# Performance work log

Measured on AMD Instinct MI355X. Metric: run time of the kernel, lower is better.

## Reference

```python
import jax, jax.numpy as jnp
import numpy as np

E = 8       # num experts
T = 1024    # num tokens
H = 1024    # hidden dim
I = 1024    # intermediate dim (per gate/up half)


def setup_inputs() -> dict:
    key = jax.random.key(0)
    k1, k2, k3, k4 = jax.random.split(key, 4)
    return {
        "hidden_states": jax.random.normal(k1, (T, H), jnp.float32),
        "router_logits": jax.random.normal(k2, (T, E), jnp.float32),
        # W13 stored pre-transposed as in the module: [E, H, 2*I]
        "W13": jax.random.normal(k3, (E, H, 2 * I), jnp.float32) * 0.02,
        # W2 stored pre-transposed: [E, I, H]
        "W2": jax.random.normal(k4, (E, I, H), jnp.float32) * 0.02,
        "top_k": 2,
    }


def reference(hidden_states, router_logits, W13, W2, top_k):
    num_experts = router_logits.shape[-1]
    # --- routing: topk_softmax (softmax over all experts, then top-k) ---
    probs = jax.nn.softmax(router_logits, axis=-1)            # [T, E]
    w, idx = jax.lax.top_k(probs, top_k)                      # [T, K]
    # renormalize=True path of moe_gather
    w = w / jnp.sum(w, axis=-1, keepdims=True)
    # combine weights per expert: [T, E]
    combine = jnp.sum(jax.nn.one_hot(idx, num_experts, dtype=w.dtype) * w[..., None], axis=1)
    # --- grouped gate-up GEMM + silu_and_mul ---
    h13 = jnp.einsum('th,ehf->tef', hidden_states, W13)       # [T, E, 2I]
    gate, up = jnp.split(h13, 2, axis=-1)                     # each [T, E, I]
    act = jax.nn.silu(gate) * up                              # silu_and_mul
    # --- grouped down GEMM ---
    down = jnp.einsum('tei,eih->teh', act, W2)                # [T, E, H]
    # --- combine (moe_gather) ---
    return jnp.einsum('te,teh->th', combine, down)            # [T, H]
```

## Files before the change

kernel.cpp:

```cpp
#include <hip/hip_runtime.h>
#include <stdint.h>

#define NE    8
#define NTOK  1024
#define NH    1024
#define NI    1024
#define N13   2048

#define PREP_BLOCKS 513
#define G1MAX       1248
#define G2MAX       1248

typedef __attribute__((ext_vector_type(8))) short short8;
typedef __attribute__((ext_vector_type(4))) float f32x4;
typedef unsigned short u16;
typedef unsigned int   u32;

__device__ __forceinline__ u16 f2bf(float x) {
    union { float f; u32 u; } v; v.f = x;
    return (u16)((v.u + 0x7fffu + ((v.u >> 16) & 1u)) >> 16);
}
__device__ __forceinline__ u32 pack2(float a, float b) {
    return (u32)f2bf(a) | ((u32)f2bf(b) << 16);
}
__device__ __forceinline__ u32 cvt_pk(float lo, float hi) {
    u32 r;
    asm("v_cvt_pk_bf16_f32 %0, %1, %2" : "=v"(r) : "v"(lo), "v"(hi));
    return r;
}
__device__ __forceinline__ void async_ld16(u16* lds, const u16* g) {
    __builtin_amdgcn_global_load_lds(
        (const __attribute__((address_space(1))) u32*)g,
        (__attribute__((address_space(3))) u32*)lds, 16, 0, 0);
}

__device__ __forceinline__ bool find_tile(
    const int* __restrict__ counts, int tile, int bm, int ntn,
    int& e_o, int& mt_o, int& nt_o, int& cnt_o, int& base_o)
{
    int base = 0;
    #pragma unroll
    for (int e = 0; e < NE; e++) {
        const int cnt = counts[e];
        const int mtiles = (cnt + bm - 1) / bm;
        const int tiles = mtiles * ntn;
        if (tile < tiles) {
            e_o = e; mt_o = tile / ntn; nt_o = tile - (tile / ntn) * ntn;
            cnt_o = cnt; base_o = base; return true;
        }
        tile -= tiles; base += cnt;
    }
    return false;
}

#define SYNCV(N)                                                           \
    {                                                                      \
        asm volatile("s_waitcnt vmcnt(" #N ") lgkmcnt(0)" ::: "memory");   \
        __builtin_amdgcn_s_barrier();                                      \
        __builtin_amdgcn_sched_barrier(0);                                 \
    }

__global__ __launch_bounds__(256) void prep_kernel(
    const float* __restrict__ X, const float* __restrict__ logits,
    int* __restrict__ counts, int* __restrict__ pair_tok,
    int* __restrict__ inv, float* __restrict__ tokw,
    u16* __restrict__ Xb)
{
    __shared__ int s_cnt[NE];
    __shared__ int s_base[NE];
    const int tid = threadIdx.x;
    const int b = blockIdx.x;

    if (b == 0) {
        if (tid < NE) s_cnt[tid] = 0;
        __syncthreads();
        int eA[4][2]; int slotA[4][2]; float wA[4][2];
        #pragma unroll
        for (int i = 0; i < 4; i++) {
            const int t = tid * 4 + i;
            float l[NE];
            #pragma unroll
            for (int e = 0; e < NE; e++) l[e] = logits[t * NE + e];
            int i0 = 0;
            #pragma unroll
            for (int e = 1; e < NE; e++) if (l[e] > l[i0]) i0 = e;
            int i1 = -1;
            #pragma unroll
            for (int e = 0; e < NE; e++) {
                if (e == i0) continue;
                if (i1 < 0 || l[e] > l[i1]) i1 = e;
            }
            const float e10 = __expf(l[i1] - l[i0]);
            const float invw = 1.0f / (1.0f + e10);
            eA[i][0] = i0; eA[i][1] = i1;
            wA[i][0] = invw; wA[i][1] = e10 * invw;
            slotA[i][0] = atomicAdd(&s_cnt[i0], 1);
            slotA[i][1] = atomicAdd(&s_cnt[i1], 1);
        }
        __syncthreads();
        if (tid == 0) {
            int acc = 0;
            #pragma unroll
            for (int e = 0; e < NE; e++) { s_base[e] = acc; acc += s_cnt[e]; }
        }
        __syncthreads();
        if (tid < NE) counts[tid] = s_cnt[tid];
        #pragma unroll
        for (int i = 0; i < 4; i++) {
            const int t = tid * 4 + i;
            #pragma unroll
            for (int k = 0; k < 2; k++) {
                const int p = s_base[eA[i][k]] + slotA[i][k];
                pair_tok[p] = t;
                inv[t * 2 + k] = p;
                tokw[t * 2 + k] = wA[i][k];
            }
        }
    } else {
        const int i = (b - 1) * 256 + tid;
        const float4* s = (const float4*)X;
        const float4 a = s[2 * i], c = s[2 * i + 1];
        uint4 o;
        o.x = pack2(a.x, a.y);
        o.y = pack2(a.z, a.w);
        o.z = pack2(c.x, c.y);
        o.w = pack2(c.z, c.w);
        *(uint4*)(Xb + (size_t)i * 8) = o;
    }
}

__global__ __launch_bounds__(256, 4) void gemm1_kernel(
    const u16* __restrict__ Xb, const float* __restrict__ W13,
    const int* __restrict__ counts, const int* __restrict__ pair_tok,
    u16* __restrict__ act)
{
    int e, mt, nt, cnt, base;
    if (!find_tile(counts, blockIdx.x, 64, 32, e, mt, nt, cnt, base)) return;

    __shared__ __align__(16) u16 As[3][64 * 32];
    __shared__ __align__(16) u16 Bs[3][64 * 40];

    const int tid = threadIdx.x;
    const int ct  = nt * 32;

    const int csrc = (((tid & 3) ^ ((tid >> 3) & 3)) << 3);
    const int arow = mt * 64 + (tid >> 2);
    const int tok  = pair_tok[base + min(arow, cnt - 1)];
    const u16* ga  = Xb + (size_t)tok * NH + csrc;

    const int n0 = (tid & 15) << 2;
    const int kp = tid >> 4;
    const int kc = kp >> 2;
    const int f0 = (n0 < 32) ? (ct + n0) : (NI + ct + n0 - 32);
    const float* gw = W13 + ((size_t)e * NH + 2 * kp) * N13 + f0;
    int wboff[4];
    #pragma unroll
    for (int jj = 0; jj < 4; jj++) {
        const int n = n0 + jj;
        wboff[jj] = n * 40 + ((kc ^ ((n >> 3) & 3)) << 3) + ((kp & 3) << 1);
    }

    const int lane = tid & 63, w = tid >> 6;
    const int quad = lane >> 4, lid = lane & 15;
    const int rw = w >> 1, cw = w & 1;
    int aoff[2];
    #pragma unroll
    for (int mi = 0; mi < 2; mi++) {
        const int r = rw * 32 + mi * 16 + lid;
        aoff[mi] = r * 32 + ((quad ^ ((r >> 1) & 3)) << 3);
    }
    int bgoff, buoff;
    { const int n = cw * 16 + lid;
      bgoff = n * 40 + ((quad ^ ((n >> 3) & 3)) << 3); }
    { const int n = 32 + cw * 16 + lid;
      buoff = n * 40 + ((quad ^ ((n >> 3) & 3)) << 3); }

    f32x4 accg[2] = {};
    f32x4 accu[2] = {};
    float4 bq[3][2];

#define ISSUEA1(S, K) async_ld16(&As[S][tid * 8], ga + (K));
#define LOADB1(RB, K)                                                      \
    { bq[RB][0] = *(const float4*)(gw + (size_t)(K) * N13);                \
      bq[RB][1] = *(const float4*)(gw + (size_t)(K) * N13 + N13); }
#define WRB1(S)                                                            \
    { _Pragma("unroll") for (int jj = 0; jj < 4; jj++) {                   \
        *(u32*)&Bs[S][wboff[jj]] =                                         \
            cvt_pk(((const float*)&bq[S][0])[jj],                          \
                   ((const float*)&bq[S][1])[jj]);                         \
    } }
#define COMP1(S)                                                           \
    {                                                                      \
        const short8 gv = *(const short8*)&Bs[S][bgoff];                   \
        const short8 uv = *(const short8*)&Bs[S][buoff];                   \
        __builtin_amdgcn_s_setprio(1);                                     \
        _Pragma("unroll") for (int mi = 0; mi < 2; mi++) {                 \
            const short8 av = *(const short8*)&As[S][aoff[mi]];            \
            accg[mi] = __builtin_amdgcn_mfma_f32_16x16x32_bf16(            \
                av, gv, accg[mi], 0, 0, 0);                                \
            accu[mi] = __builtin_amdgcn_mfma_f32_16x16x32_bf16(            \
                av, uv, accu[mi], 0, 0, 0);                                \
        }                                                                  \
        __builtin_amdgcn_s_setprio(0);                                     \
    }
#define G1_STEP(J, NV)                                                     \
    SYNCV(NV)                                                              \
    if ((J) + 2 < 32) { ISSUEA1((((J) + 2) % 3), (((J) + 2) * 32)) }       \
    if ((J) + 3 < 32) { LOADB1(((J) % 3), (((J) + 3) * 32)) }              \
    COMP1(((J) % 3))                                                       \
    if ((J) + 1 < 32) { WRB1((((J) + 1) % 3)) }

    LOADB1(0, 0)
    ISSUEA1(0, 0)
    LOADB1(1, 32)
    ISSUEA1(1, 32)
    LOADB1(2, 64)
    asm volatile("s_waitcnt vmcnt(6)" ::: "memory");
    WRB1(0)

    G1_STEP(0, 3)  G1_STEP(1, 3)  G1_STEP(2, 3)  G1_STEP(3, 3)
    G1_STEP(4, 3)  G1_STEP(5, 3)  G1_STEP(6, 3)  G1_STEP(7, 3)
    G1_STEP(8, 3)  G1_STEP(9, 3)  G1_STEP(10, 3) G1_STEP(11, 3)
    G1_STEP(12, 3) G1_STEP(13, 3) G1_STEP(14, 3) G1_STEP(15, 3)
    G1_STEP(16, 3) G1_STEP(17, 3) G1_STEP(18, 3) G1_STEP(19, 3)
    G1_STEP(20, 3) G1_STEP(21, 3) G1_STEP(22, 3) G1_STEP(23, 3)
    G1_STEP(24, 3) G1_STEP(25, 3) G1_STEP(26, 3) G1_STEP(27, 3)
    G1_STEP(28, 3) G1_STEP(29, 3) G1_STEP(30, 1) G1_STEP(31, 0)

    const int col = ct + cw * 16 + lid;
    #pragma unroll
    for (int mi = 0; mi < 2; mi++) {
        #pragma unroll
        for (int r = 0; r < 4; r++) {
            const int row = mt * 64 + rw * 32 + mi * 16 + quad * 4 + r;
            if (row < cnt) {
                const float g = accg[mi][r], u = accu[mi][r];
                act[(size_t)(base + row) * NI + col] =
                    f2bf(g / (1.0f + __expf(-g)) * u);
            }
        }
    }
#undef ISSUEA1
#undef LOADB1
#undef WRB1
#undef COMP1
#undef G1_STEP
}

__global__ __launch_bounds__(256, 4) void gemm2_kernel(
    const u16* __restrict__ act, const float* __restrict__ W2,
    const int* __restrict__ counts,
    float* __restrict__ down0, float* __restrict__ down1)
{
    int e, mt, ntq, cnt, base;
    if (!find_tile(counts, blockIdx.x, 64, 32, e, mt, ntq, cnt, base)) return;
    const int kh = ntq & 1;
    const int nt = ntq >> 1;
    const int ct = nt * 64;
    const int kbase = kh * 512;
    float* __restrict__ dwn = kh ? down1 : down0;

    __shared__ __align__(16) u16 As[3][64 * 32];
    __shared__ __align__(16) u16 Bs[3][64 * 40];

    const int tid = threadIdx.x;

    const int csrc = (((tid & 3) ^ ((tid >> 3) & 3)) << 3);
    const int arow = mt * 64 + (tid >> 2);
    const int p    = base + min(arow, cnt - 1);
    const u16* ga  = act + (size_t)p * NI + kbase + csrc;

    const int n0 = (tid & 15) << 2;
    const int kp = tid >> 4;
    const int kc = kp >> 2;
    const float* gw = W2 + ((size_t)e * NI + kbase + 2 * kp) * NH + ct + n0;
    int wboff[4];
    #pragma unroll
    for (int jj = 0; jj < 4; jj++) {
        const int n = n0 + jj;
        wboff[jj] = n * 40 + ((kc ^ ((n >> 3) & 3)) << 3) + ((kp & 3) << 1);
    }

    const int lane = tid & 63, w = tid >> 6;
    const int quad = lane >> 4, lid = lane & 15;
    const int rw = w >> 1, cw = w & 1;
    int aoff[2], boff[2];
    #pragma unroll
    for (int mi = 0; mi < 2; mi++) {
        const int r = rw * 32 + mi * 16 + lid;
        aoff[mi] = r * 32 + ((quad ^ ((r >> 1) & 3)) << 3);
    }
    #pragma unroll
    for (int nj = 0; nj < 2; nj++) {
        const int n = cw * 32 + nj * 16 + lid;
        boff[nj] = n * 40 + ((quad ^ ((n >> 3) & 3)) << 3);
    }

    f32x4 acc[2][2] = {};
    float4 bq[3][2];

#define ISSUEA2(S, K) async_ld16(&As[S][tid * 8], ga + (K));
#define LOADB2(RB, K)                                                      \
    { bq[RB][0] = *(const float4*)(gw + (size_t)(K) * NH);                 \
      bq[RB][1] = *(const float4*)(gw + (size_t)(K) * NH + NH); }
#define WRB2(S)                                                            \
    { _Pragma("unroll") for (int jj = 0; jj < 4; jj++) {                   \
        *(u32*)&Bs[S][wboff[jj]] =                                         \
            cvt_pk(((const float*)&bq[S][0])[jj],                          \
                   ((const float*)&bq[S][1])[jj]);                         \
    } }
#define COMP2(S)                                                           \
    {                                                                      \
        const short8 bv0 = *(const short8*)&Bs[S][boff[0]];                \
        const short8 bv1 = *(const short8*)&Bs[S][boff[1]];                \
        __builtin_amdgcn_s_setprio(1);                                     \
        _Pragma("unroll") for (int mi = 0; mi < 2; mi++) {                 \
            const short8 av = *(const short8*)&As[S][aoff[mi]];            \
            acc[mi][0] = __builtin_amdgcn_mfma_f32_16x16x32_bf16(          \
                av, bv0, acc[mi][0], 0, 0, 0);                             \
            acc[mi][1] = __builtin_amdgcn_mfma_f32_16x16x32_bf16(          \
                av, bv1, acc[mi][1], 0, 0, 0);                             \
        }                                                                  \
        __builtin_amdgcn_s_setprio(0);                                     \
    }
#define G2_STEP(J, NV)                                                     \
    SYNCV(NV)                                                              \
    if ((J) + 2 < 16) { ISSUEA2((((J) + 2) % 3), (((J) + 2) * 32)) }       \
    if ((J) + 3 < 16) { LOADB2(((J) % 3), (((J) + 3) * 32)) }              \
    COMP2(((J) % 3))                                                       \
    if ((J) + 1 < 16) { WRB2((((J) + 1) % 3)) }

    LOADB2(0, 0)
    ISSUEA2(0, 0)
    LOADB2(1, 32)
    ISSUEA2(1, 32)
    LOADB2(2, 64)
    asm volatile("s_waitcnt vmcnt(6)" ::: "memory");
    WRB2(0)

    G2_STEP(0, 3)  G2_STEP(1, 3)  G2_STEP(2, 3)  G2_STEP(3, 3)
    G2_STEP(4, 3)  G2_STEP(5, 3)  G2_STEP(6, 3)  G2_STEP(7, 3)
    G2_STEP(8, 3)  G2_STEP(9, 3)  G2_STEP(10, 3) G2_STEP(11, 3)
    G2_STEP(12, 3) G2_STEP(13, 3) G2_STEP(14, 1) G2_STEP(15, 0)

    #pragma unroll
    for (int mi = 0; mi < 2; mi++) {
        #pragma unroll
        for (int r = 0; r < 4; r++) {
            const int row = mt * 64 + rw * 32 + mi * 16 + quad * 4 + r;
            if (row < cnt) {
                #pragma unroll
                for (int nj = 0; nj < 2; nj++) {
                    dwn[(size_t)(base + row) * NH + ct + cw * 32 + nj * 16 + lid] =
                        acc[mi][nj][r];
                }
            }
        }
    }
#undef ISSUEA2
#undef LOADB2
#undef WRB2
#undef COMP2
#undef G2_STEP
}

__global__ __launch_bounds__(256) void combine_kernel(
    const float* __restrict__ down0, const float* __restrict__ down1,
    const int* __restrict__ inv, const float* __restrict__ tokw,
    float* __restrict__ out)
{
    const int t = blockIdx.x;
    const int p0 = inv[2 * t], p1 = inv[2 * t + 1];
    const float w0 = tokw[2 * t], w1 = tokw[2 * t + 1];
    const int i = threadIdx.x * 4;
    const float4 a0 = *(const float4*)(down0 + (size_t)p0 * NH + i);
    const float4 a1 = *(const float4*)(down1 + (size_t)p0 * NH + i);
    const float4 b0 = *(const float4*)(down0 + (size_t)p1 * NH + i);
    const float4 b1 = *(const float4*)(down1 + (size_t)p1 * NH + i);
    float4 o;
    o.x = w0 * (a0.x + a1.x) + w1 * (b0.x + b1.x);
    o.y = w0 * (a0.y + a1.y) + w1 * (b0.y + b1.y);
    o.z = w0 * (a0.z + a1.z) + w1 * (b0.z + b1.z);
    o.w = w0 * (a0.w + a1.w) + w1 * (b0.w + b1.w);
    *(float4*)(out + (size_t)t * NH + i) = o;
}

extern "C" void kernel_launch(void* const* d_in, const int* in_sizes, int n_in,
                              void* d_out, int out_size, void* d_ws, size_t ws_size,
                              hipStream_t stream)
{
    const float* X      = (const float*)d_in[0];
    const float* logits = (const float*)d_in[1];
    const float* W13    = (const float*)d_in[2];
    const float* W2     = (const float*)d_in[3];
    float* out = (float*)d_out;

    char* ws = (char*)d_ws;
    int*   counts   = (int*)(ws + 0);
    int*   pair_tok = (int*)(ws + 1024);
    int*   inv      = (int*)(ws + 16384);
    float* tokw     = (float*)(ws + 32768);
    u16*   Xb       = (u16*)(ws + 65536);
    u16*   act      = (u16*)(ws + (size_t)4  * 1024 * 1024);
    float* down0    = (float*)(ws + (size_t)8  * 1024 * 1024);
    float* down1    = (float*)(ws + (size_t)16 * 1024 * 1024);

    prep_kernel<<<PREP_BLOCKS, 256, 0, stream>>>(
        X, logits, counts, pair_tok, inv, tokw, Xb);
    gemm1_kernel<<<G1MAX, 256, 0, stream>>>(Xb, W13, counts, pair_tok, act);
    gemm2_kernel<<<G2MAX, 256, 0, stream>>>(act, W2, counts, down0, down1);
    combine_kernel<<<NTOK, 256, 0, stream>>>(down0, down1, inv, tokw, out);
}
```

Before: 187.6 us.

## Pre-convert weights to transposed bf16 in prep and stream them with async LDS loads

The prep kernel gains 6144 blocks that transpose W13 and W2 through shared memory into bf16 [E,N,K] buffers in the workspace. The GEMMs then load B tiles with global_load_lds directly, with no register-staged fp32 loads or in-loop conversion. The M tile grows from 64 to 128 rows and the pipeline deepens to four stages. Weight conversion is still done on every call, so fp32 weights are read once and bf16 copies are written and then re-read, which adds an extra pass over the weights.

Result: faster. 171.7 us (-8.4%).

```diff
diff --git a/kernel.cpp b/kernel.cpp
--- a/kernel.cpp
+++ b/kernel.cpp
@@ -7,9 +7,9 @@
 #define NI    1024
 #define N13   2048
 
-#define PREP_BLOCKS 513
-#define G1MAX       1248
-#define G2MAX       1248
+#define PREP_BLOCKS 6657
+#define G1MAX       768
+#define G2MAX       768
 
 typedef __attribute__((ext_vector_type(8))) short short8;
 typedef __attribute__((ext_vector_type(4))) float f32x4;
@@ -19,9 +19,6 @@
 __device__ __forceinline__ u16 f2bf(float x) {
     union { float f; u32 u; } v; v.f = x;
     return (u16)((v.u + 0x7fffu + ((v.u >> 16) & 1u)) >> 16);
-}
-__device__ __forceinline__ u32 pack2(float a, float b) {
-    return (u32)f2bf(a) | ((u32)f2bf(b) << 16);
 }
 __device__ __forceinline__ u32 cvt_pk(float lo, float hi) {
     u32 r;
@@ -62,16 +59,18 @@
 
 __global__ __launch_bounds__(256) void prep_kernel(
     const float* __restrict__ X, const float* __restrict__ logits,
+    const float* __restrict__ W13, const float* __restrict__ W2,
     int* __restrict__ counts, int* __restrict__ pair_tok,
     int* __restrict__ inv, float* __restrict__ tokw,
-    u16* __restrict__ Xb)
-{
-    __shared__ int s_cnt[NE];
-    __shared__ int s_base[NE];
+    u16* __restrict__ Xb, u16* __restrict__ W13t, u16* __restrict__ W2t)
+{
+    __shared__ __align__(16) float Ts[64][65];
     const int tid = threadIdx.x;
     const int b = blockIdx.x;
 
     if (b == 0) {
+        int* s_cnt  = (int*)&Ts[0][0];
+        int* s_base = s_cnt + NE;
         if (tid < NE) s_cnt[tid] = 0;
         __syncthreads();
         int eA[4][2]; int slotA[4][2]; float wA[4][2];
@@ -116,85 +115,104 @@
                 tokw[t * 2 + k] = wA[i][k];
             }
         }
-    } else {
+    } else if (b <= 512) {
         const int i = (b - 1) * 256 + tid;
         const float4* s = (const float4*)X;
         const float4 a = s[2 * i], c = s[2 * i + 1];
         uint4 o;
-        o.x = pack2(a.x, a.y);
-        o.y = pack2(a.z, a.w);
-        o.z = pack2(c.x, c.y);
-        o.w = pack2(c.z, c.w);
+        o.x = cvt_pk(a.x, a.y);
+        o.y = cvt_pk(a.z, a.w);
+        o.z = cvt_pk(c.x, c.y);
+        o.w = cvt_pk(c.z, c.w);
         *(uint4*)(Xb + (size_t)i * 8) = o;
-    }
-}
-
-__global__ __launch_bounds__(256, 4) void gemm1_kernel(
-    const u16* __restrict__ Xb, const float* __restrict__ W13,
+    } else {
+        const int wb = b - 513;
+        const float* src; u16* dst; int K, N, tb;
+        if (wb < 4096) { src = W13; dst = W13t; K = NH; N = N13; tb = wb; }
+        else           { src = W2;  dst = W2t;  K = NI; N = NH;  tb = wb - 4096; }
+        const int ktiles = K >> 6, ntiles = N >> 6;
+        const int tpe = ktiles * ntiles;
+        const int e = tb / tpe;
+        const int rem = tb - e * tpe;
+        const int kt = rem / ntiles, ntl = rem - (rem / ntiles) * ntiles;
+        const float* sb = src + ((size_t)e * K + (size_t)kt * 64) * N + ntl * 64;
+        #pragma unroll
+        for (int i = 0; i < 4; i++) {
+            const int idx = tid + i * 256;
+            const int r = idx >> 4, c = (idx & 15) << 2;
+            const float4 v = *(const float4*)(sb + (size_t)r * N + c);
+            Ts[r][c + 0] = v.x; Ts[r][c + 1] = v.y;
+            Ts[r][c + 2] = v.z; Ts[r][c + 3] = v.w;
+        }
+        __syncthreads();
+        u16* db = dst + ((size_t)e * N + (size_t)ntl * 64) * K + kt * 64;
+        #pragma unroll
+        for (int i = 0; i < 2; i++) {
+            const int u = tid + i * 256;
+            const int n = u >> 3, k8 = (u & 7) << 3;
+            uint4 o;
+            o.x = cvt_pk(Ts[k8 + 0][n], Ts[k8 + 1][n]);
+            o.y = cvt_pk(Ts[k8 + 2][n], Ts[k8 + 3][n]);
+            o.z = cvt_pk(Ts[k8 + 4][n], Ts[k8 + 5][n]);
+            o.w = cvt_pk(Ts[k8 + 6][n], Ts[k8 + 7][n]);
+            *(uint4*)(db + (size_t)n * K + k8) = o;
+        }
+    }
+}
+
+__global__ __launch_bounds__(256, 3) void gemm1_kernel(
+    const u16* __restrict__ Xb, const u16* __restrict__ W13t,
     const int* __restrict__ counts, const int* __restrict__ pair_tok,
     u16* __restrict__ act)
 {
     int e, mt, nt, cnt, base;
-    if (!find_tile(counts, blockIdx.x, 64, 32, e, mt, nt, cnt, base)) return;
-
-    __shared__ __align__(16) u16 As[3][64 * 32];
-    __shared__ __align__(16) u16 Bs[3][64 * 40];
+    if (!find_tile(counts, blockIdx.x, 128, 32, e, mt, nt, cnt, base)) return;
+
+    __shared__ __align__(16) u16 As[4][128 * 32];
+    __shared__ __align__(16) u16 Bs[4][64 * 32];
 
     const int tid = threadIdx.x;
     const int ct  = nt * 32;
 
-    const int csrc = (((tid & 3) ^ ((tid >> 3) & 3)) << 3);
-    const int arow = mt * 64 + (tid >> 2);
-    const int tok  = pair_tok[base + min(arow, cnt - 1)];
-    const u16* ga  = Xb + (size_t)tok * NH + csrc;
-
-    const int n0 = (tid & 15) << 2;
-    const int kp = tid >> 4;
-    const int kc = kp >> 2;
-    const int f0 = (n0 < 32) ? (ct + n0) : (NI + ct + n0 - 32);
-    const float* gw = W13 + ((size_t)e * NH + 2 * kp) * N13 + f0;
-    int wboff[4];
-    #pragma unroll
-    for (int jj = 0; jj < 4; jj++) {
-        const int n = n0 + jj;
-        wboff[jj] = n * 40 + ((kc ^ ((n >> 3) & 3)) << 3) + ((kp & 3) << 1);
-    }
+    const int sc = (((tid & 3) ^ ((tid >> 3) & 3)) << 3);
+    const int rr = tid >> 2;
+    const int tok0 = pair_tok[base + min(mt * 128 + rr,      cnt - 1)];
+    const int tok1 = pair_tok[base + min(mt * 128 + 64 + rr, cnt - 1)];
+    const u16* ga0 = Xb + (size_t)tok0 * NH + sc;
+    const u16* ga1 = Xb + (size_t)tok1 * NH + sc;
+    const int wcol = (rr < 32) ? (ct + rr) : (NI + ct + rr - 32);
+    const u16* gb  = W13t + ((size_t)e * N13 + wcol) * NH + sc;
 
     const int lane = tid & 63, w = tid >> 6;
     const int quad = lane >> 4, lid = lane & 15;
     const int rw = w >> 1, cw = w & 1;
-    int aoff[2];
-    #pragma unroll
-    for (int mi = 0; mi < 2; mi++) {
-        const int r = rw * 32 + mi * 16 + lid;
-        aoff[mi] = r * 32 + ((quad ^ ((r >> 1) & 3)) << 3);
+    int aoff[4];
+    #pragma unroll
+    for (int mi = 0; mi < 4; mi++) {
+        const int row = rw * 64 + mi * 16 + lid;
+        aoff[mi] = row * 32 + ((quad ^ ((row >> 1) & 3)) << 3);
     }
     int bgoff, buoff;
     { const int n = cw * 16 + lid;
-      bgoff = n * 40 + ((quad ^ ((n >> 3) & 3)) << 3); }
+      bgoff = n * 32 + ((quad ^ ((n >> 1) & 3)) << 3); }
     { const int n = 32 + cw * 16 + lid;
-      buoff = n * 40 + ((quad ^ ((n >> 3) & 3)) << 3); }
-
-    f32x4 accg[2] = {};
-    f32x4 accu[2] = {};
-    float4 bq[3][2];
-
-#define ISSUEA1(S, K) async_ld16(&As[S][tid * 8], ga + (K));
-#define LOADB1(RB, K)                                                      \
-    { bq[RB][0] = *(const float4*)(gw + (size_t)(K) * N13);                \
-      bq[RB][1] = *(const float4*)(gw + (size_t)(K) * N13 + N13); }
-#define WRB1(S)                                                            \
-    { _Pragma("unroll") for (int jj = 0; jj < 4; jj++) {                   \
-        *(u32*)&Bs[S][wboff[jj]] =                                         \
-            cvt_pk(((const float*)&bq[S][0])[jj],                          \
-                   ((const float*)&bq[S][1])[jj]);                         \
-    } }
+      buoff = n * 32 + ((quad ^ ((n >> 1) & 3)) << 3); }
+
+    f32x4 accg[4] = {};
+    f32x4 accu[4] = {};
+
+#define STAGE1(S, K)                                                       \
+    {                                                                      \
+        async_ld16(&As[S][tid * 8],         ga0 + (K));                    \
+        async_ld16(&As[S][(256 + tid) * 8], ga1 + (K));                    \
+        async_ld16(&Bs[S][tid * 8],         gb  + (K));                    \
+    }
 #define COMP1(S)                                                           \
     {                                                                      \
         const short8 gv = *(const short8*)&Bs[S][bgoff];                   \
         const short8 uv = *(const short8*)&Bs[S][buoff];                   \
         __builtin_amdgcn_s_setprio(1);                                     \
-        _Pragma("unroll") for (int mi = 0; mi < 2; mi++) {                 \
+        _Pragma("unroll") for (int mi = 0; mi < 4; mi++) {                 \
             const short8 av = *(const short8*)&As[S][aoff[mi]];            \
             accg[mi] = __builtin_amdgcn_mfma_f32_16x16x32_bf16(            \
                 av, gv, accg[mi], 0, 0, 0);                                \
@@ -203,36 +221,30 @@
         }                                                                  \
         __builtin_amdgcn_s_setprio(0);                                     \
     }
-#define G1_STEP(J, NV)                                                     \
+#define STEP1(J, NV)                                                       \
     SYNCV(NV)                                                              \
-    if ((J) + 2 < 32) { ISSUEA1((((J) + 2) % 3), (((J) + 2) * 32)) }       \
-    if ((J) + 3 < 32) { LOADB1(((J) % 3), (((J) + 3) * 32)) }              \
-    COMP1(((J) % 3))                                                       \
-    if ((J) + 1 < 32) { WRB1((((J) + 1) % 3)) }
-
-    LOADB1(0, 0)
-    ISSUEA1(0, 0)
-    LOADB1(1, 32)
-    ISSUEA1(1, 32)
-    LOADB1(2, 64)
-    asm volatile("s_waitcnt vmcnt(6)" ::: "memory");
-    WRB1(0)
-
-    G1_STEP(0, 3)  G1_STEP(1, 3)  G1_STEP(2, 3)  G1_STEP(3, 3)
-    G1_STEP(4, 3)  G1_STEP(5, 3)  G1_STEP(6, 3)  G1_STEP(7, 3)
-    G1_STEP(8, 3)  G1_STEP(9, 3)  G1_STEP(10, 3) G1_STEP(11, 3)
-    G1_STEP(12, 3) G1_STEP(13, 3) G1_STEP(14, 3) G1_STEP(15, 3)
-    G1_STEP(16, 3) G1_STEP(17, 3) G1_STEP(18, 3) G1_STEP(19, 3)
-    G1_STEP(20, 3) G1_STEP(21, 3) G1_STEP(22, 3) G1_STEP(23, 3)
-    G1_STEP(24, 3) G1_STEP(25, 3) G1_STEP(26, 3) G1_STEP(27, 3)
-    G1_STEP(28, 3) G1_STEP(29, 3) G1_STEP(30, 1) G1_STEP(31, 0)
+    if ((J) + 3 < 32) { STAGE1((((J) + 3) & 3), (((J) + 3) * 32)) }        \
+    COMP1(((J) & 3))
+
+    STAGE1(0, 0)
+    STAGE1(1, 32)
+    STAGE1(2, 64)
+
+    STEP1(0, 6)  STEP1(1, 6)  STEP1(2, 6)  STEP1(3, 6)
+    STEP1(4, 6)  STEP1(5, 6)  STEP1(6, 6)  STEP1(7, 6)
+    STEP1(8, 6)  STEP1(9, 6)  STEP1(10, 6) STEP1(11, 6)
+    STEP1(12, 6) STEP1(13, 6) STEP1(14, 6) STEP1(15, 6)
+    STEP1(16, 6) STEP1(17, 6) STEP1(18, 6) STEP1(19, 6)
+    STEP1(20, 6) STEP1(21, 6) STEP1(22, 6) STEP1(23, 6)
+    STEP1(24, 6) STEP1(25, 6) STEP1(26, 6) STEP1(27, 6)
+    STEP1(28, 6) STEP1(29, 6) STEP1(30, 3) STEP1(31, 0)
 
     const int col = ct + cw * 16 + lid;
     #pragma unroll
-    for (int mi = 0; mi < 2; mi++) {
+    for (int mi = 0; mi < 4; mi++) {
         #pragma unroll
         for (int r = 0; r < 4; r++) {
-            const int row = mt * 64 + rw * 32 + mi * 16 + quad * 4 + r;
+            const int row = mt * 128 + rw * 64 + mi * 16 + quad * 4 + r;
             if (row < cnt) {
                 const float g = accg[mi][r], u = accu[mi][r];
                 act[(size_t)(base + row) * NI + col] =
@@ -240,81 +252,66 @@
             }
         }
     }
-#undef ISSUEA1
-#undef LOADB1
-#undef WRB1
+#undef STAGE1
 #undef COMP1
-#undef G1_STEP
-}
-
-__global__ __launch_bounds__(256, 4) void gemm2_kernel(
-    const u16* __restrict__ act, const float* __restrict__ W2,
+#undef STEP1
+}
+
+__global__ __launch_bounds__(256, 3) void gemm2_kernel(
+    const u16* __restrict__ act, const u16* __restrict__ W2t,
     const int* __restrict__ counts,
     float* __restrict__ down0, float* __restrict__ down1)
 {
     int e, mt, ntq, cnt, base;
-    if (!find_tile(counts, blockIdx.x, 64, 32, e, mt, ntq, cnt, base)) return;
+    if (!find_tile(counts, blockIdx.x, 128, 32, e, mt, ntq, cnt, base)) return;
     const int kh = ntq & 1;
     const int nt = ntq >> 1;
     const int ct = nt * 64;
     const int kbase = kh * 512;
     float* __restrict__ dwn = kh ? down1 : down0;
 
-    __shared__ __align__(16) u16 As[3][64 * 32];
-    __shared__ __align__(16) u16 Bs[3][64 * 40];
+    __shared__ __align__(16) u16 As[4][128 * 32];
+    __shared__ __align__(16) u16 Bs[4][64 * 32];
 
     const int tid = threadIdx.x;
 
-    const int csrc = (((tid & 3) ^ ((tid >> 3) & 3)) << 3);
-    const int arow = mt * 64 + (tid >> 2);
-    const int p    = base + min(arow, cnt - 1);
-    const u16* ga  = act + (size_t)p * NI + kbase + csrc;
-
-    const int n0 = (tid & 15) << 2;
-    const int kp = tid >> 4;
-    const int kc = kp >> 2;
-    const float* gw = W2 + ((size_t)e * NI + kbase + 2 * kp) * NH + ct + n0;
-    int wboff[4];
-    #pragma unroll
-    for (int jj = 0; jj < 4; jj++) {
-        const int n = n0 + jj;
-        wboff[jj] = n * 40 + ((kc ^ ((n >> 3) & 3)) << 3) + ((kp & 3) << 1);
-    }
+    const int sc = (((tid & 3) ^ ((tid >> 3) & 3)) << 3);
+    const int rr = tid >> 2;
+    const int p0 = base + min(mt * 128 + rr,      cnt - 1);
+    const int p1 = base + min(mt * 128 + 64 + rr, cnt - 1);
+    const u16* ga0 = act + (size_t)p0 * NI + kbase + sc;
+    const u16* ga1 = act + (size_t)p1 * NI + kbase + sc;
+    const u16* gb  = W2t + ((size_t)e * NH + ct + rr) * NI + kbase + sc;
 
     const int lane = tid & 63, w = tid >> 6;
     const int quad = lane >> 4, lid = lane & 15;
     const int rw = w >> 1, cw = w & 1;
-    int aoff[2], boff[2];
-    #pragma unroll
-    for (int mi = 0; mi < 2; mi++) {
-        const int r = rw * 32 + mi * 16 + lid;
-        aoff[mi] = r * 32 + ((quad ^ ((r >> 1) & 3)) << 3);
+    int aoff[4], boff[2];
+    #pragma unroll
+    for (int mi = 0; mi < 4; mi++) {
+        const int row = rw * 64 + mi * 16 + lid;
+        aoff[mi] = row * 32 + ((quad ^ ((row >> 1) & 3)) << 3);
     }
     #pragma unroll
     for (int nj = 0; nj < 2; nj++) {
         const int n = cw * 32 + nj * 16 + lid;
-        boff[nj] = n * 40 + ((quad ^ ((n >> 3) & 3)) << 3);
-    }
-
-    f32x4 acc[2][2] = {};
-    float4 bq[3][2];
-
-#define ISSUEA2(S, K) async_ld16(&As[S][tid * 8], ga + (K));
-#define LOADB2(RB, K)                                                      \
-    { bq[RB][0] = *(const float4*)(gw + (size_t)(K) * NH);                 \
-      bq[RB][1] = *(const float4*)(gw + (size_t)(K) * NH + NH); }
-#define WRB2(S)                                                            \
-    { _Pragma("unroll") for (int jj = 0; jj < 4; jj++) {                   \
-        *(u32*)&Bs[S][wboff[jj]] =                                         \
-            cvt_pk(((const float*)&bq[S][0])[jj],                          \
-                   ((const float*)&bq[S][1])[jj]);                         \
-    } }
+        boff[nj] = n * 32 + ((quad ^ ((n >> 1) & 3)) << 3);
+    }
+
+    f32x4 acc[4][2] = {};
+
+#define STAGE2(S, K)                                                       \
+    {                                                                      \
+        async_ld16(&As[S][tid * 8],         ga0 + (K));                    \
+        async_ld16(&As[S][(256 + tid) * 8], ga1 + (K));                    \
+        async_ld16(&Bs[S][tid * 8],         gb  + (K));                    \
+    }
 #define COMP2(S)                                                           \
     {                                                                      \
         const short8 bv0 = *(const short8*)&Bs[S][boff[0]];                \
         const short8 bv1 = *(const short8*)&Bs[S][boff[1]];                \
         __builtin_amdgcn_s_setprio(1);                                     \
-        _Pragma("unroll") for (int mi = 0; mi < 2; mi++) {                 \
+        _Pragma("unroll") for (int mi = 0; mi < 4; mi++) {                 \
             const short8 av = *(const short8*)&As[S][aoff[mi]];            \
             acc[mi][0] = __builtin_amdgcn_mfma_f32_16x16x32_bf16(          \
                 av, bv0, acc[mi][0], 0, 0, 0);                             \
@@ -323,31 +320,25 @@
         }                                                                  \
         __builtin_amdgcn_s_setprio(0);                                     \
     }
-#define G2_STEP(J, NV)                                                     \
+#define STEP2(J, NV)                                                       \
     SYNCV(NV)                                                              \
-    if ((J) + 2 < 16) { ISSUEA2((((J) + 2) % 3), (((J) + 2) * 32)) }       \
-    if ((J) + 3 < 16) { LOADB2(((J) % 3), (((J) + 3) * 32)) }              \
-    COMP2(((J) % 3))                                                       \
-    if ((J) + 1 < 16) { WRB2((((J) + 1) % 3)) }
-
-    LOADB2(0, 0)
-    ISSUEA2(0, 0)
-    LOADB2(1, 32)
-    ISSUEA2(1, 32)
-    LOADB2(2, 64)
-    asm volatile("s_waitcnt vmcnt(6)" ::: "memory");
-    WRB2(0)
-
-    G2_STEP(0, 3)  G2_STEP(1, 3)  G2_STEP(2, 3)  G2_STEP(3, 3)
-    G2_STEP(4, 3)  G2_STEP(5, 3)  G2_STEP(6, 3)  G2_STEP(7, 3)
-    G2_STEP(8, 3)  G2_STEP(9, 3)  G2_STEP(10, 3) G2_STEP(11, 3)
-    G2_STEP(12, 3) G2_STEP(13, 3) G2_STEP(14, 1) G2_STEP(15, 0)
-
-    #pragma unroll
-    for (int mi = 0; mi < 2; mi++) {
+    if ((J) + 3 < 16) { STAGE2((((J) + 3) & 3), (((J) + 3) * 32)) }        \
+    COMP2(((J) & 3))
+
+    STAGE2(0, 0)
+    STAGE2(1, 32)
+    STAGE2(2, 64)
+
+    STEP2(0, 6)  STEP2(1, 6)  STEP2(2, 6)  STEP2(3, 6)
+    STEP2(4, 6)  STEP2(5, 6)  STEP2(6, 6)  STEP2(7, 6)
+    STEP2(8, 6)  STEP2(9, 6)  STEP2(10, 6) STEP2(11, 6)
+    STEP2(12, 6) STEP2(13, 6) STEP2(14, 3) STEP2(15, 0)
+
+    #pragma unroll
+    for (int mi = 0; mi < 4; mi++) {
         #pragma unroll
         for (int r = 0; r < 4; r++) {
-            const int row = mt * 64 + rw * 32 + mi * 16 + quad * 4 + r;
+            const int row = mt * 128 + rw * 64 + mi * 16 + quad * 4 + r;
             if (row < cnt) {
                 #pragma unroll
                 for (int nj = 0; nj < 2; nj++) {
@@ -357,11 +348,9 @@
             }
         }
     }
-#undef ISSUEA2
-#undef LOADB2
-#undef WRB2
+#undef STAGE2
 #undef COMP2
-#undef G2_STEP
+#undef STEP2
 }
 
 __global__ __launch_bounds__(256) void combine_kernel(
@@ -404,10 +393,12 @@
     u16*   act      = (u16*)(ws + (size_t)4  * 1024 * 1024);
     float* down0    = (float*)(ws + (size_t)8  * 1024 * 1024);
     float* down1    = (float*)(ws + (size_t)16 * 1024 * 1024);
+    u16*   W13t     = (u16*)(ws + (size_t)24 * 1024 * 1024);
+    u16*   W2t      = (u16*)(ws + (size_t)56 * 1024 * 1024);
 
     prep_kernel<<<PREP_BLOCKS, 256, 0, stream>>>(
-        X, logits, counts, pair_tok, inv, tokw, Xb);
-    gemm1_kernel<<<G1MAX, 256, 0, stream>>>(Xb, W13, counts, pair_tok, act);
-    gemm2_kernel<<<G2MAX, 256, 0, stream>>>(act, W2, counts, down0, down1);
+        X, logits, W13, W2, counts, pair_tok, inv, tokw, Xb, W13t, W2t);
+    gemm1_kernel<<<G1MAX, 256, 0, stream>>>(Xb, W13t, counts, pair_tok, act);
+    gemm2_kernel<<<G2MAX, 256, 0, stream>>>(act, W2t, counts, down0, down1);
     combine_kernel<<<NTOK, 256, 0, stream>>>(down0, down1, inv, tokw, out);
 }
```
